# Optimization experiments

Measured on AMD Instinct MI355X. Metric: run time of the kernel, lower is better.

Reference implementation:

```python
import jax, jax.numpy as jnp
import numpy as np

DIM = 1024
N_HEADS = 16
HEAD_DIM = DIM // N_HEADS
LORA_DIM = 16
B, T = 4, 1024


def _rope(x):
    # x: [B, H, T, D] with D even; rotate first/second halves (torch impl style)
    D = x.shape[-1]
    half = D // 2
    theta = 1.0 / (10000.0 ** (jnp.arange(0, D, 2, dtype=jnp.float32) / D))  # [D/2]
    pos = jnp.arange(x.shape[-2], dtype=jnp.float32)                         # [T]
    pt = pos[:, None] * theta[None, :]                                       # [T, D/2]
    sin, cos = jnp.sin(pt), jnp.cos(pt)
    xr, xi = x[..., :half], x[..., half:]
    return jnp.concatenate([xr * cos - xi * sin, xr * sin + xi * cos], axis=-1)


def setup_inputs() -> dict:
    key = jax.random.key(0)
    ks = jax.random.split(key, 16)
    def n(k, shape, std=0.02):
        return jax.random.normal(k, shape, jnp.float32) * std
    return {
        "x": jax.random.normal(ks[0], (B, T, DIM), jnp.float32),
        "q_w": n(ks[1], (DIM, DIM)),
        "k_w": n(ks[2], (DIM, DIM)),
        "v_w": n(ks[3], (DIM, DIM)),
        "q_a": n(ks[4], (LORA_DIM, DIM), 0.001),
        "q_b": n(ks[5], (DIM, LORA_DIM), 0.001),
        "q_l": jax.random.normal(ks[6], (DIM,), jnp.float32),
        "k_a": n(ks[7], (LORA_DIM, DIM), 0.001),
        "k_b": n(ks[8], (DIM, LORA_DIM), 0.001),
        "k_l": jax.random.normal(ks[9], (DIM,), jnp.float32),
        "v_a": n(ks[10], (LORA_DIM, DIM), 0.001),
        "v_b": n(ks[11], (DIM, LORA_DIM), 0.001),
        "v_l": jax.random.normal(ks[12], (DIM,), jnp.float32),
        "proj_w": n(ks[13], (DIM, DIM)),
        "proj_b": n(ks[14], (DIM,)),
    }


def reference(x, q_w, k_w, v_w, q_a, q_b, q_l, k_a, k_b, k_l,
              v_a, v_b, v_l, proj_w, proj_b):
    Bb, Tt, C = x.shape
    # token shift: xx[t] = x[t-1], xx[0] = 0 (ZeroPad2d((0,0,1,-1)))
    xx = jnp.pad(x, ((0, 0), (1, 0), (0, 0)))[:, :Tt]
    xxx = xx - x

    def lora(a, b, lam):
        return lam + jnp.tanh(x @ a.T) @ b.T  # [B,T,C]

    q = (x + xxx * lora(q_a, q_b, q_l)) @ q_w.T
    k = (x + xxx * lora(k_a, k_b, k_l)) @ k_w.T
    v = (x + xxx * lora(v_a, v_b, v_l)) @ v_w.T

    def split_heads(t):
        return t.reshape(Bb, Tt, N_HEADS, HEAD_DIM).transpose(0, 2, 1, 3)  # [B,H,T,D]

    q = _rope(split_heads(q))
    k = _rope(split_heads(k))
    v = split_heads(v)

    scale = 1.0 / np.sqrt(HEAD_DIM).astype(np.float32)
    scores = jnp.einsum('bhqd,bhkd->bhqk', q, k) * scale
    causal = jnp.tril(jnp.ones((Tt, Tt), dtype=bool))
    scores = jnp.where(causal, scores, jnp.float32(-1e30))
    att = jax.nn.softmax(scores, axis=-1)
    out = jnp.einsum('bhqk,bhkd->bhqd', att, v)
    out = out.transpose(0, 2, 1, 3).reshape(Bb, Tt, C)
    return out @ proj_w.T + proj_b
```

## Files before the change

### kernel.cpp

```cpp
#include <hip/hip_runtime.h>
#include <hip/hip_bf16.h>

typedef __hip_bfloat16 bf16;
typedef __attribute__((ext_vector_type(8))) short bf16x8;
typedef __attribute__((ext_vector_type(4))) float f32x4;

typedef const __attribute__((address_space(1))) unsigned int* gp_t;
typedef __attribute__((address_space(3))) unsigned int* lp_t;

__device__ __forceinline__ bf16 tobf(float f) { return __float2bfloat16(f); }
__device__ __forceinline__ float tof(bf16 h) { return __bfloat162float(h); }

__device__ __forceinline__ short bfbits(float f) {
    bf16 h = __float2bfloat16(f);
    return *reinterpret_cast<short*>(&h);
}
__device__ __forceinline__ bf16x8 pack8(float4 a, float4 b) {
    bf16x8 r;
    r[0] = bfbits(a.x); r[1] = bfbits(a.y); r[2] = bfbits(a.z); r[3] = bfbits(a.w);
    r[4] = bfbits(b.x); r[5] = bfbits(b.y); r[6] = bfbits(b.z); r[7] = bfbits(b.w);
    return r;
}

__device__ __forceinline__ void gload_lds16(const void* g, void* l) {
    __builtin_amdgcn_global_load_lds((gp_t)g, (lp_t)l, 16, 0, 0);
}

__global__ __launch_bounds__(256) void lora_gate_fused(
    const float* x,
    const float* qa, const float* ka, const float* va,
    const float* qbw, const float* ql,
    const float* kbw, const float* kl,
    const float* vbw, const float* vl,
    const float* qw, const float* kw, const float* vw, const float* pw,
    bf16* wdst,
    bf16* xqo, bf16* xko, bf16* xvo) {
    const int XS = 1028;
    int row0 = blockIdx.x * 8;
    int t0 = row0 & 1023;
    int tid = threadIdx.x;
    int wave = tid >> 6, lane = tid & 63;
    int quad = lane >> 4, l16 = lane & 15;

    __shared__ float sx[9 * 1028];
    __shared__ float spT[3][4][8][17];
    __shared__ float sT[8 * 48];

    {
        int prow = (row0 == 0) ? 0 : row0 - 1;
        for (int i = 0; i < 9; ++i) {
            int grow = (i == 0) ? prow : row0 + i - 1;
            gload_lds16(x + (size_t)grow * 1024 + wave * 256 + lane * 4,
                        &sx[i * XS + wave * 256]);
        }
    }
    {
        int m = blockIdx.x >> 7;
        const float* src = m == 0 ? qw : (m == 1 ? kw : (m == 2 ? vw : pw));
        bf16* dst = wdst + (size_t)m * (1u << 20);
        int off = (blockIdx.x & 127) * 8192;
#pragma unroll
        for (int u = 0; u < 8; ++u) {
            int i = off + u * 1024 + tid * 4;
            float4 f = *(const float4*)(src + i);
            ushort4 o4;
            o4.x = (unsigned short)bfbits(f.x);
            o4.y = (unsigned short)bfbits(f.y);
            o4.z = (unsigned short)bfbits(f.z);
            o4.w = (unsigned short)bfbits(f.w);
            *(ushort4*)&dst[i] = o4;
        }
    }
    __syncthreads();

    {
        int xr = (l16 < 8) ? l16 : 7;
        f32x4 acc[3];
#pragma unroll
        for (int m = 0; m < 3; m++) acc[m] = (f32x4){0.f, 0.f, 0.f, 0.f};
        int kb = wave * 256;
#pragma unroll
        for (int kk = 0; kk < 256; kk += 32) {
            int k0 = kb + kk;
            const float* xs = &sx[(1 + xr) * XS + k0 + quad * 8];
            bf16x8 af = pack8(*(const float4*)xs, *(const float4*)(xs + 4));
#pragma unroll
            for (int m = 0; m < 3; m++) {
                const float* am = m == 0 ? qa : (m == 1 ? ka : va);
                const float* as = am + (size_t)l16 * 1024 + k0 + quad * 8;
                bf16x8 bf_ = pack8(*(const float4*)as, *(const float4*)(as + 4));
                acc[m] = __builtin_amdgcn_mfma_f32_16x16x32_bf16(af, bf_, acc[m], 0, 0, 0);
            }
        }
#pragma unroll
        for (int m = 0; m < 3; m++)
#pragma unroll
            for (int r = 0; r < 4; r++) {
                int row = quad * 4 + r;
                if (row < 8) spT[m][wave][row][l16] = acc[m][r];
            }
    }
    __syncthreads();
    if (tid < 384) {
        int m = tid >> 7, idx = tid & 127;
        int row = idx >> 4, col = idx & 15;
        float v = spT[m][0][row][col] + spT[m][1][row][col]
                + spT[m][2][row][col] + spT[m][3][row][col];
        sT[row * 48 + m * 16 + col] = tanhf(v);
    }
    __syncthreads();

#pragma unroll
    for (int u = 0; u < 4; ++u) {
        int d = tid + u * 256;
        float qbv[16], kbv[16], vbv[16];
#pragma unroll
        for (int p = 0; p < 4; ++p) {
            *(float4*)&qbv[p * 4] = *(const float4*)(qbw + (size_t)d * 16 + p * 4);
            *(float4*)&kbv[p * 4] = *(const float4*)(kbw + (size_t)d * 16 + p * 4);
            *(float4*)&vbv[p * 4] = *(const float4*)(vbw + (size_t)d * 16 + p * 4);
        }
        float qlv = ql[d], klv = kl[d], vlv = vl[d];
        float xp = (t0 == 0) ? 0.f : sx[0 * XS + d];
        for (int rr = 0; rr < 8; ++rr) {
            float xc = sx[(rr + 1) * XS + d];
            float dx = xp - xc;
            float gq = qlv, gk = klv, gv = vlv;
#pragma unroll
            for (int j = 0; j < 16; ++j) {
                gq += sT[rr * 48 + j] * qbv[j];
                gk += sT[rr * 48 + 16 + j] * kbv[j];
                gv += sT[rr * 48 + 32 + j] * vbv[j];
            }
            size_t o = (size_t)(row0 + rr) * 1024 + d;
            xqo[o] = tobf(xc + dx * gq);
            xko[o] = tobf(xc + dx * gk);
            xvo[o] = tobf(xc + dx * gv);
            xp = xc;
        }
    }
}

__global__ __launch_bounds__(256) void gemm128(
    const bf16* A0, const bf16* A1, const bf16* A2,
    const bf16* W0, const bf16* W1, const bf16* W2,
    bf16* C0, bf16* C1, bf16* C2,
    const float* bias, float* outF, int proj, int zcnt) {
    const int K = 1024;
    int ppx = (zcnt * 32) >> 3;
    int xcd = blockIdx.x & 7;
    int j = blockIdx.x >> 3;
    int pair = xcd * ppx + (j >> 3);
    int n0 = (j & 7) * 128;
    int bz = pair >> 5;
    int m0 = (pair & 31) * 128;

    const bf16* A = bz == 0 ? A0 : (bz == 1 ? A1 : A2);
    const bf16* W = bz == 0 ? W0 : (bz == 1 ? W1 : W2);
    bf16* C = bz == 0 ? C0 : (bz == 1 ? C1 : C2);

    __shared__ alignas(16) bf16 sA[64 * 64];
    __shared__ alignas(16) bf16 sB[64 * 64];

    int wave = threadIdx.x >> 6, lane = threadIdx.x & 63;
    int quad = lane >> 4, l16 = lane & 15;

    f32x4 acc[4][4];
#pragma unroll
    for (int i = 0; i < 4; i++)
#pragma unroll
        for (int j2 = 0; j2 < 4; j2++) acc[i][j2] = (f32x4){0.f, 0.f, 0.f, 0.f};

    int Rb0 = wave * 16 + (lane >> 3);
    int s0 = lane & 7;

    auto stage = [&](int k0) {
#pragma unroll
        for (int p = 0; p < 2; p++) {
            int R = Rb0 + p * 8;
            int cs = s0 ^ (R & 7);
            int mr = 2 * R + (cs >> 2);
            int kc = (cs & 3) * 8;
            gload_lds16(A + (size_t)(m0 + mr) * K + k0 + kc, &sA[(wave * 16 + p * 8) * 64]);
            gload_lds16(W + (size_t)(n0 + mr) * K + k0 + kc, &sB[(wave * 16 + p * 8) * 64]);
        }
    };

    int mw = (wave >> 1) * 64, nw = (wave & 1) * 64;
    int slot = (((l16 & 1) << 2) | quad) ^ ((l16 >> 1) & 7);
    int abase = ((mw >> 1) + (l16 >> 1)) * 64 + slot * 8;
    int bbase = ((nw >> 1) + (l16 >> 1)) * 64 + slot * 8;

    for (int it = 0; it < 32; ++it) {
        __syncthreads();
        stage(it * 32);
        __syncthreads();
        bf16x8 af[4], bfr[4];
#pragma unroll
        for (int f = 0; f < 4; f++) {
            af[f] = *(const bf16x8*)&sA[abase + f * 512];
            bfr[f] = *(const bf16x8*)&sB[bbase + f * 512];
        }
#pragma unroll
        for (int i = 0; i < 4; i++)
#pragma unroll
            for (int j2 = 0; j2 < 4; j2++)
                acc[i][j2] = __builtin_amdgcn_mfma_f32_16x16x32_bf16(af[i], bfr[j2], acc[i][j2], 0, 0, 0);
    }

    if (proj) {
#pragma unroll
        for (int i = 0; i < 4; i++) {
            int mrow = m0 + mw + i * 16 + quad * 4;
#pragma unroll
            for (int j2 = 0; j2 < 4; j2++) {
                int col = n0 + nw + j2 * 16 + l16;
                float bv = bias[col];
#pragma unroll
                for (int r = 0; r < 4; r++)
                    outF[(size_t)(mrow + r) * 1024 + col] = acc[i][j2][r] + bv;
            }
        }
    } else if (bz < 2) {
        float sc = (bz == 0) ? 0.125f : 1.0f;
        int tb = ((m0 + mw) & 1023) + quad * 4;
#pragma unroll
        for (int j2 = 0; j2 < 2; j2++) {
            int d = j2 * 16 + l16;
            float theta = __expf(-(float)d * (9.210340371976184f / 32.0f));
            float s1, c1, s16, c16, st, ct;
            sincosf(theta, &s1, &c1);
            sincosf(16.0f * theta, &s16, &c16);
            sincosf((float)tb * theta, &st, &ct);
            int col = n0 + nw + j2 * 16 + l16;
#pragma unroll
            for (int i = 0; i < 4; i++) {
                int mrow = m0 + mw + i * 16 + quad * 4;
                float c = ct, s = st;
#pragma unroll
                for (int r = 0; r < 4; r++) {
                    float xr = acc[i][j2][r], xi = acc[i][j2 + 2][r];
                    C[(size_t)(mrow + r) * 1024 + col] = tobf((xr * c - xi * s) * sc);
                    C[(size_t)(mrow + r) * 1024 + col + 32] = tobf((xr * s + xi * c) * sc);
                    float cn = c * c1 - s * s1;
                    s = s * c1 + c * s1;
                    c = cn;
                }
                float cn = ct * c16 - st * s16;
                st = st * c16 + ct * s16;
                ct = cn;
            }
        }
    } else {
#pragma unroll
        for (int i = 0; i < 4; i++) {
            int mrow = m0 + mw + i * 16 + quad * 4;
#pragma unroll
            for (int j2 = 0; j2 < 4; j2++) {
                int col = n0 + nw + j2 * 16 + l16;
                ushort4 o4;
                o4.x = (unsigned short)bfbits(acc[i][j2][0]);
                o4.y = (unsigned short)bfbits(acc[i][j2][1]);
                o4.z = (unsigned short)bfbits(acc[i][j2][2]);
                o4.w = (unsigned short)bfbits(acc[i][j2][3]);
                *(ushort4*)&C[(size_t)col * 4096 + mrow] = o4;
            }
        }
    }
}

__global__ __launch_bounds__(256) void attention(const bf16* Qm, const bf16* Km,
                                                 const bf16* Vt, bf16* attn) {
    int gid = blockIdx.x;
    int qblk = 15 - (gid >> 6);
    int bh = (((gid >> 3) & 7) << 3) | (gid & 7);
    int b = bh >> 4, h = bh & 15;
    int wave = threadIdx.x >> 6, lane = threadIdx.x & 63;
    int quad = lane >> 4, l16 = lane & 15;
    int m7 = l16 & 7;

    const bf16* Qb = Qm + (size_t)b * 1024 * 1024 + h * 64;
    const bf16* Kb = Km + (size_t)b * 1024 * 1024 + h * 64;
    const bf16* Vb = Vt + (size_t)(h * 64) * 4096 + b * 1024;

    __shared__ alignas(16) bf16 sK[2][64 * 64];
    __shared__ alignas(16) bf16 sV[2][64 * 64];
    __shared__ alignas(16) bf16 sP[4][16 * 64];

    int srow = lane >> 3;
    int scol = ((lane & 7) ^ srow) * 8;

    auto stage = [&](int kt, int bufi) {
#pragma unroll
        for (int p = 0; p < 2; p++) {
            int rbase = p * 32 + wave * 8;
            gload_lds16(Kb + (size_t)(kt * 64 + rbase + srow) * 1024 + scol, &sK[bufi][rbase * 64]);
            gload_lds16(Vb + (size_t)(rbase + srow) * 4096 + kt * 64 + scol, &sV[bufi][rbase * 64]);
        }
    };

    int qrow0 = qblk * 64 + wave * 16;
    bf16x8 aq0 = *(const bf16x8*)&Qb[(size_t)(qrow0 + l16) * 1024 + quad * 8];
    bf16x8 aq1 = *(const bf16x8*)&Qb[(size_t)(qrow0 + l16) * 1024 + quad * 8 + 32];

    f32x4 o[4];
#pragma unroll
    for (int nt = 0; nt < 4; nt++) o[nt] = (f32x4){0.f, 0.f, 0.f, 0.f};
    float lpart[4] = {0.f, 0.f, 0.f, 0.f};

    stage(0, 0);

    int buf = 0;
    for (int kt = 0; kt <= qblk; ++kt, buf ^= 1) {
        __syncthreads();
        if (kt < qblk) stage(kt + 1, buf ^ 1);

        f32x4 S[4];
#pragma unroll
        for (int j = 0; j < 4; j++) {
            int row = j * 16 + l16;
            bf16x8 bk0 = *(const bf16x8*)&sK[buf][row * 64 + ((quad ^ m7) * 8)];
            bf16x8 bk1 = *(const bf16x8*)&sK[buf][row * 64 + (((quad + 4) ^ m7) * 8)];
            f32x4 z = __builtin_amdgcn_mfma_f32_16x16x32_bf16(aq0, bk0, (f32x4){0.f, 0.f, 0.f, 0.f}, 0, 0, 0);
            S[j] = __builtin_amdgcn_mfma_f32_16x16x32_bf16(aq1, bk1, z, 0, 0, 0);
        }
        if (kt == qblk) {
#pragma unroll
            for (int j = 0; j < 4; j++) {
                int key = kt * 64 + j * 16 + l16;
#pragma unroll
                for (int r = 0; r < 4; r++) {
                    int qr = qrow0 + quad * 4 + r;
                    if (key > qr) S[j][r] = -3.0e38f;
                }
            }
        }
#pragma unroll
        for (int j = 0; j < 4; j++)
#pragma unroll
            for (int r = 0; r < 4; r++) {
                float p = __expf(S[j][r]);
                S[j][r] = p;
                lpart[r] += p;
            }

#pragma unroll
        for (int j = 0; j < 4; j++) {
            int c = j * 2 + (l16 >> 3);
#pragma unroll
            for (int r = 0; r < 4; r++) {
                int prow = quad * 4 + r;
                sP[wave][prow * 64 + ((c ^ (prow & 7)) * 8) + m7] = tobf(S[j][r]);
            }
        }
        asm volatile("s_waitcnt lgkmcnt(0)" ::: "memory");
        bf16x8 ap0 = *(const bf16x8*)&sP[wave][l16 * 64 + ((quad ^ m7) * 8)];
        bf16x8 ap1 = *(const bf16x8*)&sP[wave][l16 * 64 + (((quad + 4) ^ m7) * 8)];
#pragma unroll
        for (int nt = 0; nt < 4; nt++) {
            int row = nt * 16 + l16;
            bf16x8 bv0 = *(const bf16x8*)&sV[buf][row * 64 + ((quad ^ m7) * 8)];
            bf16x8 bv1 = *(const bf16x8*)&sV[buf][row * 64 + (((quad + 4) ^ m7) * 8)];
            o[nt] = __builtin_amdgcn_mfma_f32_16x16x32_bf16(ap0, bv0, o[nt], 0, 0, 0);
            o[nt] = __builtin_amdgcn_mfma_f32_16x16x32_bf16(ap1, bv1, o[nt], 0, 0, 0);
        }
    }

    float invl[4];
#pragma unroll
    for (int r = 0; r < 4; r++) {
        float v = lpart[r];
        v += __shfl_xor(v, 1);
        v += __shfl_xor(v, 2);
        v += __shfl_xor(v, 4);
        v += __shfl_xor(v, 8);
        invl[r] = 1.0f / v;
    }
#pragma unroll
    for (int nt = 0; nt < 4; nt++)
#pragma unroll
        for (int r = 0; r < 4; r++) {
            int t = qrow0 + quad * 4 + r;
            int col = h * 64 + nt * 16 + l16;
            attn[(size_t)(b * 1024 + t) * 1024 + col] = tobf(o[nt][r] * invl[r]);
        }
}

extern "C" void kernel_launch(void* const* d_in, const int* in_sizes, int n_in,
                              void* d_out, int out_size, void* d_ws, size_t ws_size,
                              hipStream_t stream) {
    const float* x = (const float*)d_in[0];
    const float* qw = (const float*)d_in[1];
    const float* kw = (const float*)d_in[2];
    const float* vw = (const float*)d_in[3];
    const float* qa = (const float*)d_in[4];
    const float* qb = (const float*)d_in[5];
    const float* ql = (const float*)d_in[6];
    const float* ka = (const float*)d_in[7];
    const float* kb = (const float*)d_in[8];
    const float* kl = (const float*)d_in[9];
    const float* va = (const float*)d_in[10];
    const float* vb = (const float*)d_in[11];
    const float* vl = (const float*)d_in[12];
    const float* pw = (const float*)d_in[13];
    const float* pb = (const float*)d_in[14];
    float* out = (float*)d_out;

    char* ws = (char*)d_ws;
    const size_t MB = 1024 * 1024;
    bf16* wqb = (bf16*)ws;
    bf16* wkb = wqb + 1048576;
    bf16* wvb = wkb + 1048576;
    bf16* wpb = wvb + 1048576;
    bf16* xqb = (bf16*)(ws + 8 * MB);
    bf16* xkb = xqb + 4194304;
    bf16* xvb = xkb + 4194304;
    bf16* qm = (bf16*)(ws + 32 * MB);
    bf16* km = qm + 4194304;
    bf16* Vt = km + 4194304;
    bf16* attn = xqb;

    lora_gate_fused<<<512, 256, 0, stream>>>(x, qa, ka, va, qb, ql, kb, kl, vb, vl,
                                             qw, kw, vw, pw, wqb,
                                             xqb, xkb, xvb);
    gemm128<<<768, 256, 0, stream>>>(xqb, xkb, xvb, wqb, wkb, wvb, qm, km, Vt,
                                     nullptr, nullptr, 0, 3);
    attention<<<1024, 256, 0, stream>>>(qm, km, Vt, attn);
    gemm128<<<256, 256, 0, stream>>>(attn, nullptr, nullptr, wpb, nullptr, nullptr,
                                     nullptr, nullptr, nullptr, pb, out, 1, 1);
}
```

Measured before the change: 204.5 us.

## Split fused LoRA gate kernel into tanh-projection and gate/convert kernels

Splits the single fused kernel into two launches. The first computes the tanh LoRA projections into a small workspace buffer. The second applies the gates while reading x directly from global memory, and uses separate blocks for the weight bf16 conversion. This removes the roughly 37 KB shared-memory staging of x and the serial dependence between weight conversion and gate compute, aiming for higher occupancy and more parallel blocks. The cost is an extra kernel launch, a global round trip for T, and uncoalesced-free but uncached repeated reads of x.

```diff
diff --git a/kernel.cpp b/kernel.cpp
--- a/kernel.cpp
+++ b/kernel.cpp
@@ -26,39 +26,68 @@
     __builtin_amdgcn_global_load_lds((gp_t)g, (lp_t)l, 16, 0, 0);
 }
 
-__global__ __launch_bounds__(256) void lora_gate_fused(
-    const float* x,
-    const float* qa, const float* ka, const float* va,
+__global__ __launch_bounds__(256) void lora_T(
+    const float* x, const float* qa, const float* ka, const float* va,
+    float* T) {
+    int row0 = blockIdx.x * 8;
+    int tid = threadIdx.x;
+    int wave = tid >> 6, lane = tid & 63;
+    int quad = lane >> 4, l16 = lane & 15;
+
+    __shared__ float spT[3][4][8][17];
+
+    int xr = row0 + ((l16 < 8) ? l16 : 7);
+    f32x4 acc[3];
+#pragma unroll
+    for (int m = 0; m < 3; m++) acc[m] = (f32x4){0.f, 0.f, 0.f, 0.f};
+    int kb = wave * 256;
+#pragma unroll
+    for (int kk = 0; kk < 256; kk += 32) {
+        int k0 = kb + kk;
+        const float* xs = x + (size_t)xr * 1024 + k0 + quad * 8;
+        bf16x8 af = pack8(*(const float4*)xs, *(const float4*)(xs + 4));
+#pragma unroll
+        for (int m = 0; m < 3; m++) {
+            const float* am = m == 0 ? qa : (m == 1 ? ka : va);
+            const float* as = am + (size_t)l16 * 1024 + k0 + quad * 8;
+            bf16x8 bf_ = pack8(*(const float4*)as, *(const float4*)(as + 4));
+            acc[m] = __builtin_amdgcn_mfma_f32_16x16x32_bf16(af, bf_, acc[m], 0, 0, 0);
+        }
+    }
+#pragma unroll
+    for (int m = 0; m < 3; m++)
+#pragma unroll
+        for (int r = 0; r < 4; r++) {
+            int row = quad * 4 + r;
+            if (row < 8) spT[m][wave][row][l16] = acc[m][r];
+        }
+    __syncthreads();
+    for (int i3 = tid; i3 < 384; i3 += 256) {
+        int m = i3 >> 7, idx = i3 & 127;
+        int row = idx >> 4, col = idx & 15;
+        float v = spT[m][0][row][col] + spT[m][1][row][col]
+                + spT[m][2][row][col] + spT[m][3][row][col];
+        T[(size_t)(row0 + row) * 48 + m * 16 + col] = tanhf(v);
+    }
+}
+
+__global__ __launch_bounds__(256) void gate_conv(
+    const float* x, const float* T,
     const float* qbw, const float* ql,
     const float* kbw, const float* kl,
     const float* vbw, const float* vl,
     const float* qw, const float* kw, const float* vw, const float* pw,
     bf16* wdst,
     bf16* xqo, bf16* xko, bf16* xvo) {
-    const int XS = 1028;
-    int row0 = blockIdx.x * 8;
-    int t0 = row0 & 1023;
+    int bid = blockIdx.x;
     int tid = threadIdx.x;
-    int wave = tid >> 6, lane = tid & 63;
-    int quad = lane >> 4, l16 = lane & 15;
-
-    __shared__ float sx[9 * 1028];
-    __shared__ float spT[3][4][8][17];
-    __shared__ float sT[8 * 48];
-
-    {
-        int prow = (row0 == 0) ? 0 : row0 - 1;
-        for (int i = 0; i < 9; ++i) {
-            int grow = (i == 0) ? prow : row0 + i - 1;
-            gload_lds16(x + (size_t)grow * 1024 + wave * 256 + lane * 4,
-                        &sx[i * XS + wave * 256]);
-        }
-    }
-    {
-        int m = blockIdx.x >> 7;
+
+    if (bid >= 512) {
+        int cb = bid - 512;
+        int m = cb >> 7;
         const float* src = m == 0 ? qw : (m == 1 ? kw : (m == 2 ? vw : pw));
         bf16* dst = wdst + (size_t)m * (1u << 20);
-        int off = (blockIdx.x & 127) * 8192;
+        int off = (cb & 127) * 8192;
 #pragma unroll
         for (int u = 0; u < 8; ++u) {
             int i = off + u * 1024 + tid * 4;
@@ -70,44 +99,13 @@
             o4.w = (unsigned short)bfbits(f.w);
             *(ushort4*)&dst[i] = o4;
         }
-    }
-    __syncthreads();
-
-    {
-        int xr = (l16 < 8) ? l16 : 7;
-        f32x4 acc[3];
-#pragma unroll
-        for (int m = 0; m < 3; m++) acc[m] = (f32x4){0.f, 0.f, 0.f, 0.f};
-        int kb = wave * 256;
-#pragma unroll
-        for (int kk = 0; kk < 256; kk += 32) {
-            int k0 = kb + kk;
-            const float* xs = &sx[(1 + xr) * XS + k0 + quad * 8];
-            bf16x8 af = pack8(*(const float4*)xs, *(const float4*)(xs + 4));
-#pragma unroll
-            for (int m = 0; m < 3; m++) {
-                const float* am = m == 0 ? qa : (m == 1 ? ka : va);
-                const float* as = am + (size_t)l16 * 1024 + k0 + quad * 8;
-                bf16x8 bf_ = pack8(*(const float4*)as, *(const float4*)(as + 4));
-                acc[m] = __builtin_amdgcn_mfma_f32_16x16x32_bf16(af, bf_, acc[m], 0, 0, 0);
-            }
-        }
-#pragma unroll
-        for (int m = 0; m < 3; m++)
-#pragma unroll
-            for (int r = 0; r < 4; r++) {
-                int row = quad * 4 + r;
-                if (row < 8) spT[m][wave][row][l16] = acc[m][r];
-            }
-    }
-    __syncthreads();
-    if (tid < 384) {
-        int m = tid >> 7, idx = tid & 127;
-        int row = idx >> 4, col = idx & 15;
-        float v = spT[m][0][row][col] + spT[m][1][row][col]
-                + spT[m][2][row][col] + spT[m][3][row][col];
-        sT[row * 48 + m * 16 + col] = tanhf(v);
-    }
+        return;
+    }
+
+    int row0 = bid * 8;
+    int t0 = row0 & 1023;
+    __shared__ float sT[8 * 48];
+    for (int i = tid; i < 384; i += 256) sT[i] = T[(size_t)row0 * 48 + i];
     __syncthreads();
 
 #pragma unroll
@@ -121,9 +119,9 @@
             *(float4*)&vbv[p * 4] = *(const float4*)(vbw + (size_t)d * 16 + p * 4);
         }
         float qlv = ql[d], klv = kl[d], vlv = vl[d];
-        float xp = (t0 == 0) ? 0.f : sx[0 * XS + d];
+        float xp = (t0 == 0) ? 0.f : x[(size_t)(row0 - 1) * 1024 + d];
         for (int rr = 0; rr < 8; ++rr) {
-            float xc = sx[(rr + 1) * XS + d];
+            float xc = x[(size_t)(row0 + rr) * 1024 + d];
             float dx = xp - xc;
             float gq = qlv, gk = klv, gv = vlv;
 #pragma unroll
@@ -418,11 +416,12 @@
     bf16* qm = (bf16*)(ws + 32 * MB);
     bf16* km = qm + 4194304;
     bf16* Vt = km + 4194304;
+    float* T = (float*)(ws + 32 * MB);
     bf16* attn = xqb;
 
-    lora_gate_fused<<<512, 256, 0, stream>>>(x, qa, ka, va, qb, ql, kb, kl, vb, vl,
-                                             qw, kw, vw, pw, wqb,
-                                             xqb, xkb, xvb);
+    lora_T<<<512, 256, 0, stream>>>(x, qa, ka, va, T);
+    gate_conv<<<1024, 256, 0, stream>>>(x, T, qb, ql, kb, kl, vb, vl,
+                                        qw, kw, vw, pw, wqb, xqb, xkb, xvb);
     gemm128<<<768, 256, 0, stream>>>(xqb, xkb, xvb, wqb, wkb, wvb, qm, km, Vt,
                                      nullptr, nullptr, 0, 3);
     attention<<<1024, 256, 0, stream>>>(qm, km, Vt, attn);
```

New measurement: 212.0 us. 3.6% more time.
